# Optimization experiments

Measured on AMD Instinct MI355X. Metric: run time of the kernel, lower is better.

Reference implementation:

```python
import jax, jax.numpy as jnp
import numpy as np

WH, WW = 8, 8          # window size
SH, SW = 4, 4          # shift size
HEADS = 8

def _rel_pos_index(wh, ww):
    # static Swin relative-position index, identical to the torch __init__ math
    coords = np.stack(np.meshgrid(np.arange(wh), np.arange(ww), indexing='ij')).reshape(2, -1)
    rel = (coords[:, :, None] - coords[:, None, :]).transpose(1, 2, 0)
    rel[..., 0] += wh - 1
    rel[..., 1] += ww - 1
    rel[..., 0] *= 2 * ww - 1
    return jnp.asarray(rel.sum(-1))  # (N, N) int

REL_IDX = _rel_pos_index(WH, WW)

def _ln(x, w, b, eps=1e-5):
    m = x.mean(-1, keepdims=True)
    v = ((x - m) ** 2).mean(-1, keepdims=True)
    return (x - m) * jax.lax.rsqrt(v + eps) * w + b

def _lin(x, w, b):  # torch Linear convention: w is (out, in)
    return jnp.einsum('...i,oi->...o', x, w) + b

def _partition(x):
    B, H, W, C = x.shape
    x = x.reshape(B, H // WH, WH, W // WW, WW, C).transpose(0, 1, 3, 2, 4, 5)
    return x.reshape(-1, WH * WW, C)  # (B*nW, N, C)

def _reverse(w, B, H, W):
    C = w.shape[-1]
    x = w.reshape(B, H // WH, W // WW, WH, WW, C).transpose(0, 1, 3, 2, 4, 5)
    return x.reshape(B, H, W, C)

def _win_attn(q_in, kv_in, qw, qb, kvw, kvb, pw, pb, table, mask):
    B_, N1, C = q_in.shape
    N2 = kv_in.shape[1]
    hd = C // HEADS
    scale = hd ** -0.5
    q = _lin(q_in, qw, qb).reshape(B_, N1, HEADS, hd).transpose(0, 2, 1, 3)
    kv = _lin(kv_in, kvw, kvb).reshape(B_, N2, 2, HEADS, hd).transpose(2, 0, 3, 1, 4)
    k, v = kv[0], kv[1]
    attn = jnp.einsum('bhqd,bhkd->bhqk', q * scale, k)               # (B_, H, N1, N2)
    bias = table[REL_IDX.reshape(-1)].reshape(N1, N2, HEADS).transpose(2, 0, 1)
    attn = attn + bias[None]
    nW = mask.shape[0]
    attn = attn.reshape(B_ // nW, nW, HEADS, N1, N2) + mask[None, :, None]
    attn = jax.nn.softmax(attn.reshape(B_, HEADS, N1, N2), axis=-1)
    out = jnp.einsum('bhqk,bhkd->bhqd', attn, v).transpose(0, 2, 1, 3).reshape(B_, N1, C)
    return _lin(out, pw, pb)

def reference(x, attn_kv, mask_q, mask_qkv,
              n1w, n1b, n2w, n2b, n3w, n3b, nkvw, nkvb,
              a1_qw, a1_qb, a1_kvw, a1_kvb, a1_pw, a1_pb, a1_tab,
              a2_qw, a2_qb, a2_kvw, a2_kvb, a2_pw, a2_pb, a2_tab,
              fc1w, fc1b, fc2w, fc2b):
    B, H, W, C = x.shape  # H,W divisible by window -> pad is a no-op; shift active
    # --- shifted-window self attention ---
    shortcut = x
    h = jnp.roll(_ln(x, n1w, n1b), (-SH, -SW), axis=(1, 2))
    w = _win_attn(_partition(h), _partition(h), a1_qw, a1_qb, a1_kvw, a1_kvb,
                  a1_pw, a1_pb, a1_tab, mask_q)
    x = shortcut + jnp.roll(_reverse(w, B, H, W), (SH, SW), axis=(1, 2))
    # --- shifted-window cross attention ---
    shortcut = x
    hq = jnp.roll(_ln(x, n2w, n2b), (-SH, -SW), axis=(1, 2))
    hkv = jnp.roll(_ln(attn_kv, nkvw, nkvb), (-SH, -SW), axis=(1, 2))
    w = _win_attn(_partition(hq), _partition(hkv), a2_qw, a2_qb, a2_kvw, a2_kvb,
                  a2_pw, a2_pb, a2_tab, mask_qkv)
    x = shortcut + jnp.roll(_reverse(w, B, H, W), (SH, SW), axis=(1, 2))
    # --- MLP ---
    h = _ln(x, n3w, n3b)
    h = _lin(jax.nn.gelu(_lin(h, fc1w, fc1b), approximate=False), fc2w, fc2b)
    return x + h

def setup_inputs() -> dict:
    key = jax.random.key(0)
    ks = jax.random.split(key, 20)
    B, H, W, C = 2, 256, 256, 256
    nW = (H // WH) * (W // WW)
    N = WH * WW
    hid = 4 * C
    tab = (2 * WH - 1) * (2 * WW - 1)
    rn = lambda k, s, sd=0.02: jax.random.normal(k, s, jnp.float32) * sd
    shift_mask = lambda k: jnp.where(jax.random.uniform(k, (nW, N, N)) > 0.1, 0.0, -100.0).astype(jnp.float32)
    return dict(
        x=jax.random.normal(ks[0], (B, H, W, C), jnp.float32),
        attn_kv=jax.random.normal(ks[1], (B, H, W, C), jnp.float32),
        mask_q=shift_mask(ks[2]), mask_qkv=shift_mask(ks[3]),
        n1w=jnp.ones((C,)), n1b=jnp.zeros((C,)),
        n2w=jnp.ones((C,)), n2b=jnp.zeros((C,)),
        n3w=jnp.ones((C,)), n3b=jnp.zeros((C,)),
        nkvw=jnp.ones((C,)), nkvb=jnp.zeros((C,)),
        a1_qw=rn(ks[4], (C, C)), a1_qb=jnp.zeros((C,)),
        a1_kvw=rn(ks[5], (2 * C, C)), a1_kvb=jnp.zeros((2 * C,)),
        a1_pw=rn(ks[6], (C, C)), a1_pb=jnp.zeros((C,)),
        a1_tab=rn(ks[7], (tab, HEADS)),
        a2_qw=rn(ks[8], (C, C)), a2_qb=jnp.zeros((C,)),
        a2_kvw=rn(ks[9], (2 * C, C)), a2_kvb=jnp.zeros((2 * C,)),
        a2_pw=rn(ks[10], (C, C)), a2_pb=jnp.zeros((C,)),
        a2_tab=rn(ks[11], (tab, HEADS)),
        fc1w=rn(ks[12], (hid, C)), fc1b=jnp.zeros((hid,)),
        fc2w=rn(ks[13], (C, hid)), fc2b=jnp.zeros((C,)),
    )
```

## Files before the change

kernel.cpp:

```cpp
#include <hip/hip_runtime.h>
#include <math.h>

typedef __attribute__((ext_vector_type(8))) short short8;
typedef __attribute__((ext_vector_type(4))) float f32x4;

__device__ __forceinline__ unsigned short f2bf(float f) {
  unsigned u = __float_as_uint(f);
  u += 0x7FFFu + ((u >> 16) & 1u);
  return (unsigned short)(u >> 16);
}
__device__ __forceinline__ float bf2f(unsigned short h) {
  return __uint_as_float(((unsigned)h) << 16);
}

static constexpr unsigned OFF_WQKV1 = 0;
static constexpr unsigned OFF_BQKV1 = 393216;
static constexpr unsigned OFF_WQ2   = 396288;
static constexpr unsigned OFF_BQ2   = 527360;
static constexpr unsigned OFF_WKV2  = 528384;
static constexpr unsigned OFF_BKV2  = 790528;
static constexpr unsigned OFF_WP1   = 792576;
static constexpr unsigned OFF_BP1   = 923648;
static constexpr unsigned OFF_WP2   = 924672;
static constexpr unsigned OFF_BP2   = 1055744;
static constexpr unsigned OFF_WFC1  = 1056768;
static constexpr unsigned OFF_BFC1  = 1581056;
static constexpr unsigned OFF_WFC2  = 1585152;
static constexpr unsigned OFF_BFC2  = 2109440;
static constexpr unsigned OFF_BIAS1 = 2110464;
static constexpr unsigned OFF_BIAS2 = 2241536;

static constexpr size_t OFF_X1  = 4194304;
static constexpr size_t OFF_QKV = OFF_X1  + 134217728ull;
static constexpr size_t OFF_KV2 = OFF_QKV + 67108864ull;
static constexpr size_t OFF_HB  = OFF_QKV + 201326592ull;
static constexpr size_t OFF_HA  = OFF_HB  + 67108864ull;

__global__ __launch_bounds__(256) void prep_kernel(
    const float* __restrict__ a1_qw, const float* __restrict__ a1_qb,
    const float* __restrict__ a1_kvw, const float* __restrict__ a1_kvb,
    const float* __restrict__ a1_pw, const float* __restrict__ a1_pb,
    const float* __restrict__ a1_tab,
    const float* __restrict__ a2_qw, const float* __restrict__ a2_qb,
    const float* __restrict__ a2_kvw, const float* __restrict__ a2_kvb,
    const float* __restrict__ a2_pw, const float* __restrict__ a2_pb,
    const float* __restrict__ a2_tab,
    const float* __restrict__ fc1w, const float* __restrict__ fc1b,
    const float* __restrict__ fc2w, const float* __restrict__ fc2b,
    char* __restrict__ ws)
{
  int idx = blockIdx.x * 256 + threadIdx.x;
  const float SC = 0.17677669529663687f;
  if (idx < 196608) {
    int o = idx >> 8, c = idx & 255;
    float v = (o < 256) ? a1_qw[o * 256 + c] * SC : a1_kvw[(o - 256) * 256 + c];
    ((unsigned short*)(ws + OFF_WQKV1))[idx] = f2bf(v);
    return;
  }
  idx -= 196608;
  if (idx < 768) {
    float v = (idx < 256) ? a1_qb[idx] * SC : a1_kvb[idx - 256];
    ((float*)(ws + OFF_BQKV1))[idx] = v; return;
  }
  idx -= 768;
  if (idx < 65536) { ((unsigned short*)(ws + OFF_WQ2))[idx] = f2bf(a2_qw[idx] * SC); return; }
  idx -= 65536;
  if (idx < 256)   { ((float*)(ws + OFF_BQ2))[idx] = a2_qb[idx] * SC; return; }
  idx -= 256;
  if (idx < 131072){ ((unsigned short*)(ws + OFF_WKV2))[idx] = f2bf(a2_kvw[idx]); return; }
  idx -= 131072;
  if (idx < 512)   { ((float*)(ws + OFF_BKV2))[idx] = a2_kvb[idx]; return; }
  idx -= 512;
  if (idx < 65536) { ((unsigned short*)(ws + OFF_WP1))[idx] = f2bf(a1_pw[idx]); return; }
  idx -= 65536;
  if (idx < 256)   { ((float*)(ws + OFF_BP1))[idx] = a1_pb[idx]; return; }
  idx -= 256;
  if (idx < 65536) { ((unsigned short*)(ws + OFF_WP2))[idx] = f2bf(a2_pw[idx]); return; }
  idx -= 65536;
  if (idx < 256)   { ((float*)(ws + OFF_BP2))[idx] = a2_pb[idx]; return; }
  idx -= 256;
  if (idx < 262144){ ((unsigned short*)(ws + OFF_WFC1))[idx] = f2bf(fc1w[idx]); return; }
  idx -= 262144;
  if (idx < 1024)  { ((float*)(ws + OFF_BFC1))[idx] = fc1b[idx]; return; }
  idx -= 1024;
  if (idx < 262144){ ((unsigned short*)(ws + OFF_WFC2))[idx] = f2bf(fc2w[idx]); return; }
  idx -= 262144;
  if (idx < 256)   { ((float*)(ws + OFF_BFC2))[idx] = fc2b[idx]; return; }
  idx -= 256;
  if (idx < 32768) {
    int h = idx >> 12, r = idx & 4095;
    int i = r >> 6, j = r & 63;
    int rel = ((i >> 3) - (j >> 3) + 7) * 15 + ((i & 7) - (j & 7) + 7);
    ((float*)(ws + OFF_BIAS1))[idx] = a1_tab[rel * 8 + h];
    return;
  }
  idx -= 32768;
  if (idx < 32768) {
    int h = idx >> 12, r = idx & 4095;
    int i = r >> 6, j = r & 63;
    int rel = ((i >> 3) - (j >> 3) + 7) * 15 + ((i & 7) - (j & 7) + 7);
    ((float*)(ws + OFF_BIAS2))[idx] = a2_tab[rel * 8 + h];
  }
}

template<int SHIFTED>
__global__ __launch_bounds__(256)
void ln_kernel(const float* __restrict__ in, const float* __restrict__ gw,
               const float* __restrict__ gb, unsigned short* __restrict__ out)
{
  const int token = blockIdx.x * 4 + (threadIdx.x >> 6);
  const int lane  = threadIdx.x & 63;
  const float4 v = *(const float4*)&in[token * 256 + lane * 4];
  float s  = v.x + v.y + v.z + v.w;
  float sq = v.x * v.x + v.y * v.y + v.z * v.z + v.w * v.w;
  #pragma unroll
  for (int m = 1; m < 64; m <<= 1) { s += __shfl_xor(s, m, 64); sq += __shfl_xor(sq, m, 64); }
  const float mean = s * 0.00390625f;
  const float var  = sq * 0.00390625f - mean * mean;
  const float rstd = rsqrtf(var + 1e-5f);
  const float4 wv = *(const float4*)&gw[lane * 4];
  const float4 bv = *(const float4*)&gb[lane * 4];
  int orow;
  if (SHIFTED) {
    const int bb = token >> 16;
    const int h  = (token >> 8) & 255;
    const int w  = token & 255;
    const int hs  = (h - 4) & 255;
    const int wsn = (w - 4) & 255;
    orow = (((bb << 10) + ((hs >> 3) << 5) + (wsn >> 3)) << 6) + ((hs & 7) << 3) + (wsn & 7);
  } else {
    orow = token;
  }
  ushort4 o;
  o.x = f2bf((v.x - mean) * rstd * wv.x + bv.x);
  o.y = f2bf((v.y - mean) * rstd * wv.y + bv.y);
  o.z = f2bf((v.z - mean) * rstd * wv.z + bv.z);
  o.w = f2bf((v.w - mean) * rstd * wv.w + bv.w);
  *(ushort4*)&out[orow * 256 + lane * 4] = o;
}

template<int MODE>
__global__ __launch_bounds__(256)
void gemm_bt(const unsigned short* __restrict__ A, const unsigned short* __restrict__ W,
             const float* __restrict__ bias, int M, int N, int K,
             unsigned short* __restrict__ outB, float* outF, const float* resF)
{
  __shared__ unsigned short As[128 * 64];
  __shared__ unsigned short Bs[128 * 64];
  const int tid  = threadIdx.x;
  const int lane = tid & 63;
  const int wv   = tid >> 6;
  const int n0 = blockIdx.x * 128;
  const int m0 = blockIdx.y * 128;
  const int wm = (wv >> 1) * 64;
  const int wn = (wv & 1) * 64;
  const int lr = lane & 15;
  const int lk = (lane >> 4) * 8;

  f32x4 acc[4][4] = {};

  for (int k0 = 0; k0 < K; k0 += 64) {
    #pragma unroll
    for (int s = 0; s < 4; s++) {
      const int u = tid + s * 256;
      const int r = u >> 3;
      const int c = (u & 7) * 8;
      const int sw = (r & 7) << 3;
      *(short8*)&As[(r * 64 + c) ^ sw] = *(const short8*)&A[(m0 + r) * K + k0 + c];
      *(short8*)&Bs[(r * 64 + c) ^ sw] = *(const short8*)&W[(n0 + r) * K + k0 + c];
    }
    __syncthreads();
    #pragma unroll
    for (int kk = 0; kk < 64; kk += 32) {
      short8 af[4], bf[4];
      #pragma unroll
      for (int i = 0; i < 4; i++) {
        const int ra = wm + i * 16 + lr;
        const int rb = wn + i * 16 + lr;
        af[i] = *(const short8*)&As[(ra * 64 + kk + lk) ^ ((ra & 7) << 3)];
        bf[i] = *(const short8*)&Bs[(rb * 64 + kk + lk) ^ ((rb & 7) << 3)];
      }
      #pragma unroll
      for (int i = 0; i < 4; i++)
        #pragma unroll
        for (int j = 0; j < 4; j++)
          acc[i][j] = __builtin_amdgcn_mfma_f32_16x16x32_bf16(af[i], bf[j], acc[i][j], 0, 0, 0);
    }
    __syncthreads();
  }

  #pragma unroll
  for (int j = 0; j < 4; j++) {
    const int col = n0 + wn + j * 16 + lr;
    const float bv = bias[col];
    #pragma unroll
    for (int i = 0; i < 4; i++) {
      #pragma unroll
      for (int r = 0; r < 4; r++) {
        const int row = m0 + wm + i * 16 + (lane >> 4) * 4 + r;
        float v = acc[i][j][r] + bv;
        if (MODE == 0) {
          outB[row * N + col] = f2bf(v);
        } else if (MODE == 1) {
          float g = 0.5f * v * (1.0f + erff(v * 0.70710678118654752f));
          outB[row * N + col] = f2bf(g);
        } else if (MODE == 2) {
          const int i6 = row & 63, wn_ = row >> 6;
          const int bb = wn_ >> 10, wi = wn_ & 1023;
          const int hs  = ((wi >> 5) << 3) + (i6 >> 3);
          const int wsn = ((wi & 31) << 3) + (i6 & 7);
          const int hh = (hs + 4) & 255, ww = (wsn + 4) & 255;
          const int nat = (bb << 16) + (hh << 8) + ww;
          outF[nat * 256 + col] = resF[nat * 256 + col] + v;
        } else {
          outF[row * N + col] = resF[row * N + col] + v;
        }
      }
    }
  }
}

__global__ __launch_bounds__(256)
void attn_kernel(const unsigned short* __restrict__ Qm, int sq,
                 const unsigned short* __restrict__ Km,
                 const unsigned short* __restrict__ Vm, int skv,
                 const float* __restrict__ mask, const float* __restrict__ biasT,
                 unsigned short* __restrict__ outO)
{
  __shared__ unsigned short Kl[64 * 256];
  __shared__ unsigned short Vl[64 * 256];
  const int win = blockIdx.x;
  const int wi  = win & 1023;
  const int tid = threadIdx.x;
  const int t = tid & 63;
  const int g = tid >> 6;

  for (int u = tid; u < 2048; u += 256) {
    const int j = u >> 5;
    const int c = (u & 31) * 8;
    *(short8*)&Kl[j * 256 + c] = *(const short8*)&Km[(win * 64 + j) * skv + c];
    *(short8*)&Vl[j * 256 + c] = *(const short8*)&Vm[(win * 64 + j) * skv + c];
  }
  __syncthreads();

  const float* mrow = &mask[wi * 4096 + t * 64];

  #pragma unroll
  for (int hh = 0; hh < 2; hh++) {
    const int h = g * 2 + hh;
    float qr[32];
    const unsigned short* qp = &Qm[(win * 64 + t) * sq + h * 32];
    #pragma unroll
    for (int c = 0; c < 4; c++) {
      const short8 qv = *(const short8*)&qp[c * 8];
      #pragma unroll
      for (int e = 0; e < 8; e++) qr[c * 8 + e] = bf2f((unsigned short)qv[e]);
    }
    const float* brow = &biasT[h * 4096 + t * 64];
    float s[64];
    #pragma unroll
    for (int j = 0; j < 64; j++) {
      const unsigned short* kp = &Kl[j * 256 + h * 32];
      float a = 0.f;
      #pragma unroll
      for (int c = 0; c < 4; c++) {
        const short8 k8 = *(const short8*)&kp[c * 8];
        #pragma unroll
        for (int e = 0; e < 8; e++) a = fmaf(qr[c * 8 + e], bf2f((unsigned short)k8[e]), a);
      }
      s[j] = a + brow[j] + mrow[j];
    }
    float mx = -1e30f;
    #pragma unroll
    for (int j = 0; j < 64; j++) mx = fmaxf(mx, s[j]);
    float sum = 0.f;
    #pragma unroll
    for (int j = 0; j < 64; j++) { const float e = __expf(s[j] - mx); s[j] = e; sum += e; }
    const float inv = 1.f / sum;
    float o[32];
    #pragma unroll
    for (int d = 0; d < 32; d++) o[d] = 0.f;
    #pragma unroll
    for (int j = 0; j < 64; j++) {
      const float p = s[j];
      const unsigned short* vp = &Vl[j * 256 + h * 32];
      #pragma unroll
      for (int c = 0; c < 4; c++) {
        const short8 v8 = *(const short8*)&vp[c * 8];
        #pragma unroll
        for (int e = 0; e < 8; e++) o[c * 8 + e] = fmaf(p, bf2f((unsigned short)v8[e]), o[c * 8 + e]);
      }
    }
    unsigned short* op = &outO[(win * 64 + t) * 256 + h * 32];
    #pragma unroll
    for (int c = 0; c < 4; c++) {
      short8 ov;
      #pragma unroll
      for (int e = 0; e < 8; e++) ov[e] = (short)f2bf(o[c * 8 + e] * inv);
      *(short8*)&op[c * 8] = ov;
    }
  }
}

extern "C" void kernel_launch(void* const* d_in, const int* in_sizes, int n_in,
                              void* d_out, int out_size, void* d_ws, size_t ws_size,
                              hipStream_t stream)
{
  const float* x       = (const float*)d_in[0];
  const float* akv     = (const float*)d_in[1];
  const float* mask_q  = (const float*)d_in[2];
  const float* mask_kv = (const float*)d_in[3];
  const float* n1w = (const float*)d_in[4];
  const float* n1b = (const float*)d_in[5];
  const float* n2w = (const float*)d_in[6];
  const float* n2b = (const float*)d_in[7];
  const float* n3w = (const float*)d_in[8];
  const float* n3b = (const float*)d_in[9];
  const float* nkvw = (const float*)d_in[10];
  const float* nkvb = (const float*)d_in[11];

  char* ws = (char*)d_ws;
  const unsigned short* WQKV1 = (const unsigned short*)(ws + OFF_WQKV1);
  const float*          BQKV1 = (const float*)(ws + OFF_BQKV1);
  const unsigned short* WQ2   = (const unsigned short*)(ws + OFF_WQ2);
  const float*          BQ2   = (const float*)(ws + OFF_BQ2);
  const unsigned short* WKV2  = (const unsigned short*)(ws + OFF_WKV2);
  const float*          BKV2  = (const float*)(ws + OFF_BKV2);
  const unsigned short* WP1   = (const unsigned short*)(ws + OFF_WP1);
  const float*          BP1   = (const float*)(ws + OFF_BP1);
  const unsigned short* WP2   = (const unsigned short*)(ws + OFF_WP2);
  const float*          BP2   = (const float*)(ws + OFF_BP2);
  const unsigned short* WFC1  = (const unsigned short*)(ws + OFF_WFC1);
  const float*          BFC1  = (const float*)(ws + OFF_BFC1);
  const unsigned short* WFC2  = (const unsigned short*)(ws + OFF_WFC2);
  const float*          BFC2  = (const float*)(ws + OFF_BFC2);
  const float* BIAS1 = (const float*)(ws + OFF_BIAS1);
  const float* BIAS2 = (const float*)(ws + OFF_BIAS2);

  float*          x1  = (float*)(ws + OFF_X1);
  unsigned short* qkv = (unsigned short*)(ws + OFF_QKV);
  unsigned short* kv2 = (unsigned short*)(ws + OFF_KV2);
  unsigned short* hB  = (unsigned short*)(ws + OFF_HB);
  unsigned short* hA  = (unsigned short*)(ws + OFF_HA);
  float* out = (float*)d_out;

  prep_kernel<<<4365, 256, 0, stream>>>(
      (const float*)d_in[12], (const float*)d_in[13], (const float*)d_in[14], (const float*)d_in[15],
      (const float*)d_in[16], (const float*)d_in[17], (const float*)d_in[18],
      (const float*)d_in[19], (const float*)d_in[20], (const float*)d_in[21], (const float*)d_in[22],
      (const float*)d_in[23], (const float*)d_in[24], (const float*)d_in[25],
      (const float*)d_in[26], (const float*)d_in[27], (const float*)d_in[28], (const float*)d_in[29],
      ws);

  ln_kernel<1><<<32768, 256, 0, stream>>>(x, n1w, n1b, hA);
  gemm_bt<0><<<dim3(6, 1024), 256, 0, stream>>>(hA, WQKV1, BQKV1, 131072, 768, 256, qkv, nullptr, nullptr);
  attn_kernel<<<2048, 256, 0, stream>>>(qkv, 768, qkv + 256, qkv + 512, 768, mask_q, BIAS1, hA);
  gemm_bt<2><<<dim3(2, 1024), 256, 0, stream>>>(hA, WP1, BP1, 131072, 256, 256, nullptr, x1, x);

  ln_kernel<1><<<32768, 256, 0, stream>>>(x1, n2w, n2b, hA);
  ln_kernel<1><<<32768, 256, 0, stream>>>(akv, nkvw, nkvb, hB);
  gemm_bt<0><<<dim3(2, 1024), 256, 0, stream>>>(hA, WQ2, BQ2, 131072, 256, 256, qkv, nullptr, nullptr);
  gemm_bt<0><<<dim3(4, 1024), 256, 0, stream>>>(hB, WKV2, BKV2, 131072, 512, 256, kv2, nullptr, nullptr);
  attn_kernel<<<2048, 256, 0, stream>>>(qkv, 256, kv2, kv2 + 256, 512, mask_kv, BIAS2, hA);
  gemm_bt<2><<<dim3(2, 1024), 256, 0, stream>>>(hA, WP2, BP2, 131072, 256, 256, nullptr, out, x1);

  ln_kernel<0><<<32768, 256, 0, stream>>>(out, n3w, n3b, hA);
  gemm_bt<1><<<dim3(8, 1024), 256, 0, stream>>>(hA, WFC1, BFC1, 131072, 1024, 256, qkv, nullptr, nullptr);
  gemm_bt<3><<<dim3(2, 1024), 256, 0, stream>>>(qkv, WFC2, BFC2, 131072, 256, 1024, nullptr, out, out);
}
```

Baseline: 2.386 ms.

## Use MFMA for window attention and direct global-to-LDS loads in GEMM

Rewrites the window attention kernel so QK^T and PV run on bf16 MFMA instructions instead of per-thread scalar FMA loops. Heads are processed in two halves, with K staged via global_load_lds, V transposed into swizzled LDS, and softmax done with cross-lane shuffles and P written to LDS as bf16. The GEMM tile loads switch to direct global-to-LDS loads with an XOR swizzle applied on the global side, and indexing is widened to size_t. Quantizing P to bf16 adds some rounding error, and the extra LDS and sync per half may limit occupancy.

```diff
diff --git a/kernel.cpp b/kernel.cpp
--- a/kernel.cpp
+++ b/kernel.cpp
@@ -11,6 +11,10 @@
 }
 __device__ __forceinline__ float bf2f(unsigned short h) {
   return __uint_as_float(((unsigned)h) << 16);
+}
+__device__ __forceinline__ void gload_lds16(const unsigned short* g, unsigned short* l) {
+  __builtin_amdgcn_global_load_lds((const __attribute__((address_space(1))) void*)g,
+                                   (__attribute__((address_space(3))) void*)l, 16, 0, 0);
 }
 
 static constexpr unsigned OFF_WQKV1 = 0;
@@ -110,7 +114,7 @@
 {
   const int token = blockIdx.x * 4 + (threadIdx.x >> 6);
   const int lane  = threadIdx.x & 63;
-  const float4 v = *(const float4*)&in[token * 256 + lane * 4];
+  const float4 v = *(const float4*)&in[(size_t)token * 256 + lane * 4];
   float s  = v.x + v.y + v.z + v.w;
   float sq = v.x * v.x + v.y * v.y + v.z * v.z + v.w * v.w;
   #pragma unroll
@@ -136,7 +140,7 @@
   o.y = f2bf((v.y - mean) * rstd * wv.y + bv.y);
   o.z = f2bf((v.z - mean) * rstd * wv.z + bv.z);
   o.w = f2bf((v.w - mean) * rstd * wv.w + bv.w);
-  *(ushort4*)&out[orow * 256 + lane * 4] = o;
+  *(ushort4*)&out[(size_t)orow * 256 + lane * 4] = o;
 }
 
 template<int MODE>
@@ -145,8 +149,8 @@
              const float* __restrict__ bias, int M, int N, int K,
              unsigned short* __restrict__ outB, float* outF, const float* resF)
 {
-  __shared__ unsigned short As[128 * 64];
-  __shared__ unsigned short Bs[128 * 64];
+  __shared__ __align__(16) unsigned short As[128 * 64];
+  __shared__ __align__(16) unsigned short Bs[128 * 64];
   const int tid  = threadIdx.x;
   const int lane = tid & 63;
   const int wv   = tid >> 6;
@@ -157,17 +161,17 @@
   const int lr = lane & 15;
   const int lk = (lane >> 4) * 8;
 
+  const int r8  = lane >> 3;
+  const int gch = (lane & 7) ^ r8;
+
   f32x4 acc[4][4] = {};
 
   for (int k0 = 0; k0 < K; k0 += 64) {
     #pragma unroll
     for (int s = 0; s < 4; s++) {
-      const int u = tid + s * 256;
-      const int r = u >> 3;
-      const int c = (u & 7) * 8;
-      const int sw = (r & 7) << 3;
-      *(short8*)&As[(r * 64 + c) ^ sw] = *(const short8*)&A[(m0 + r) * K + k0 + c];
-      *(short8*)&Bs[(r * 64 + c) ^ sw] = *(const short8*)&W[(n0 + r) * K + k0 + c];
+      const int rbase = wv * 32 + s * 8;
+      gload_lds16(&A[(size_t)(m0 + rbase + r8) * K + k0 + gch * 8], &As[rbase * 64]);
+      gload_lds16(&W[(size_t)(n0 + rbase + r8) * K + k0 + gch * 8], &Bs[rbase * 64]);
     }
     __syncthreads();
     #pragma unroll
@@ -200,20 +204,20 @@
         const int row = m0 + wm + i * 16 + (lane >> 4) * 4 + r;
         float v = acc[i][j][r] + bv;
         if (MODE == 0) {
-          outB[row * N + col] = f2bf(v);
+          outB[(size_t)row * N + col] = f2bf(v);
         } else if (MODE == 1) {
-          float g = 0.5f * v * (1.0f + erff(v * 0.70710678118654752f));
-          outB[row * N + col] = f2bf(g);
+          float gl = 0.5f * v * (1.0f + erff(v * 0.70710678118654752f));
+          outB[(size_t)row * N + col] = f2bf(gl);
         } else if (MODE == 2) {
           const int i6 = row & 63, wn_ = row >> 6;
           const int bb = wn_ >> 10, wi = wn_ & 1023;
           const int hs  = ((wi >> 5) << 3) + (i6 >> 3);
           const int wsn = ((wi & 31) << 3) + (i6 & 7);
           const int hh = (hs + 4) & 255, ww = (wsn + 4) & 255;
-          const int nat = (bb << 16) + (hh << 8) + ww;
+          const size_t nat = ((size_t)bb << 16) + (hh << 8) + ww;
           outF[nat * 256 + col] = resF[nat * 256 + col] + v;
         } else {
-          outF[row * N + col] = resF[row * N + col] + v;
+          outF[(size_t)row * N + col] = resF[(size_t)row * N + col] + v;
         }
       }
     }
@@ -227,78 +231,124 @@
                  const float* __restrict__ mask, const float* __restrict__ biasT,
                  unsigned short* __restrict__ outO)
 {
-  __shared__ unsigned short Kl[64 * 256];
-  __shared__ unsigned short Vl[64 * 256];
+  __shared__ __align__(16) unsigned short Kh[64 * 128];
+  __shared__ __align__(16) unsigned short Vth[128 * 64];
+  __shared__ __align__(16) unsigned short Ps[4 * 64 * 64];
+
   const int win = blockIdx.x;
   const int wi  = win & 1023;
   const int tid = threadIdx.x;
-  const int t = tid & 63;
-  const int g = tid >> 6;
-
-  for (int u = tid; u < 2048; u += 256) {
-    const int j = u >> 5;
-    const int c = (u & 31) * 8;
-    *(short8*)&Kl[j * 256 + c] = *(const short8*)&Km[(win * 64 + j) * skv + c];
-    *(short8*)&Vl[j * 256 + c] = *(const short8*)&Vm[(win * 64 + j) * skv + c];
-  }
-  __syncthreads();
-
-  const float* mrow = &mask[wi * 4096 + t * 64];
-
-  #pragma unroll
-  for (int hh = 0; hh < 2; hh++) {
-    const int h = g * 2 + hh;
-    float qr[32];
-    const unsigned short* qp = &Qm[(win * 64 + t) * sq + h * 32];
-    #pragma unroll
-    for (int c = 0; c < 4; c++) {
-      const short8 qv = *(const short8*)&qp[c * 8];
-      #pragma unroll
-      for (int e = 0; e < 8; e++) qr[c * 8 + e] = bf2f((unsigned short)qv[e]);
-    }
-    const float* brow = &biasT[h * 4096 + t * 64];
-    float s[64];
-    #pragma unroll
-    for (int j = 0; j < 64; j++) {
-      const unsigned short* kp = &Kl[j * 256 + h * 32];
-      float a = 0.f;
-      #pragma unroll
-      for (int c = 0; c < 4; c++) {
-        const short8 k8 = *(const short8*)&kp[c * 8];
-        #pragma unroll
-        for (int e = 0; e < 8; e++) a = fmaf(qr[c * 8 + e], bf2f((unsigned short)k8[e]), a);
-      }
-      s[j] = a + brow[j] + mrow[j];
-    }
-    float mx = -1e30f;
-    #pragma unroll
-    for (int j = 0; j < 64; j++) mx = fmaxf(mx, s[j]);
-    float sum = 0.f;
-    #pragma unroll
-    for (int j = 0; j < 64; j++) { const float e = __expf(s[j] - mx); s[j] = e; sum += e; }
-    const float inv = 1.f / sum;
-    float o[32];
-    #pragma unroll
-    for (int d = 0; d < 32; d++) o[d] = 0.f;
-    #pragma unroll
-    for (int j = 0; j < 64; j++) {
-      const float p = s[j];
-      const unsigned short* vp = &Vl[j * 256 + h * 32];
-      #pragma unroll
-      for (int c = 0; c < 4; c++) {
-        const short8 v8 = *(const short8*)&vp[c * 8];
-        #pragma unroll
-        for (int e = 0; e < 8; e++) o[c * 8 + e] = fmaf(p, bf2f((unsigned short)v8[e]), o[c * 8 + e]);
-      }
-    }
-    unsigned short* op = &outO[(win * 64 + t) * 256 + h * 32];
-    #pragma unroll
-    for (int c = 0; c < 4; c++) {
-      short8 ov;
-      #pragma unroll
-      for (int e = 0; e < 8; e++) ov[e] = (short)f2bf(o[c * 8 + e] * inv);
-      *(short8*)&op[c * 8] = ov;
-    }
+  const int lane = tid & 63;
+  const int wv  = tid >> 6;
+  const int lr = lane & 15;
+  const int g  = lane >> 4;
+  unsigned short* Pw = &Ps[wv * 4096];
+
+  for (int half = 0; half < 2; half++) {
+    {
+      const int r_off = g;
+      const int ch    = lane & 15;
+      #pragma unroll
+      for (int s = 0; s < 4; s++) {
+        const int row = wv * 16 + s * 4 + r_off;
+        const int sch = ch ^ (row & 7);
+        gload_lds16(&Km[(size_t)(win * 64 + row) * skv + half * 128 + sch * 8],
+                    &Kh[(wv * 16 + s * 4) * 128]);
+      }
+    }
+    #pragma unroll
+    for (int it = 0; it < 4; it++) {
+      const int slot = tid + it * 256;
+      const int tok = slot >> 4;
+      const int ch  = slot & 15;
+      const short8 v8 = *(const short8*)&Vm[(size_t)(win * 64 + tok) * skv + half * 128 + ch * 8];
+      #pragma unroll
+      for (int es = 0; es < 8; es++) {
+        const int e  = (es + ch) & 7;
+        const int fr = ch * 8 + e;
+        Vth[fr * 64 + (((tok >> 3) ^ (fr & 7)) << 3) + (tok & 7)] = (unsigned short)v8[e];
+      }
+    }
+    __syncthreads();
+
+    const int h = half * 4 + wv;
+    short8 af[4];
+    #pragma unroll
+    for (int i = 0; i < 4; i++)
+      af[i] = *(const short8*)&Qm[(size_t)(win * 64 + i * 16 + lr) * sq + h * 32 + g * 8];
+    f32x4 acc[4][4] = {};
+    #pragma unroll
+    for (int j = 0; j < 4; j++) {
+      const int row = j * 16 + lr;
+      const int chn = ((h & 3) * 4 + g) ^ (row & 7);
+      const short8 bf = *(const short8*)&Kh[row * 128 + chn * 8];
+      #pragma unroll
+      for (int i = 0; i < 4; i++)
+        acc[i][j] = __builtin_amdgcn_mfma_f32_16x16x32_bf16(af[i], bf, acc[i][j], 0, 0, 0);
+    }
+
+    const float* bh = &biasT[h * 4096];
+    const float* mh = &mask[(size_t)wi * 4096];
+    #pragma unroll
+    for (int i = 0; i < 4; i++) {
+      #pragma unroll
+      for (int r = 0; r < 4; r++) {
+        const int row = i * 16 + g * 4 + r;
+        #pragma unroll
+        for (int j = 0; j < 4; j++) {
+          const int col = j * 16 + lr;
+          acc[i][j][r] += bh[row * 64 + col] + mh[row * 64 + col];
+        }
+        float m4 = fmaxf(fmaxf(acc[i][0][r], acc[i][1][r]), fmaxf(acc[i][2][r], acc[i][3][r]));
+        #pragma unroll
+        for (int mk = 1; mk < 16; mk <<= 1) m4 = fmaxf(m4, __shfl_xor(m4, mk, 64));
+        float sum = 0.f;
+        #pragma unroll
+        for (int j = 0; j < 4; j++) {
+          const float e = __expf(acc[i][j][r] - m4);
+          acc[i][j][r] = e; sum += e;
+        }
+        #pragma unroll
+        for (int mk = 1; mk < 16; mk <<= 1) sum += __shfl_xor(sum, mk, 64);
+        const float inv = 1.f / sum;
+        #pragma unroll
+        for (int j = 0; j < 4; j++) {
+          const int col = j * 16 + lr;
+          Pw[row * 64 + (((col >> 3) ^ (row & 7)) << 3) + (col & 7)] = f2bf(acc[i][j][r] * inv);
+        }
+      }
+    }
+
+    f32x4 o[4][2] = {};
+    #pragma unroll
+    for (int kk = 0; kk < 2; kk++) {
+      short8 bv[2];
+      #pragma unroll
+      for (int jj = 0; jj < 2; jj++) {
+        const int frow = (h & 3) * 32 + jj * 16 + lr;
+        const int chn = (kk * 4 + g) ^ (frow & 7);
+        bv[jj] = *(const short8*)&Vth[frow * 64 + chn * 8];
+      }
+      #pragma unroll
+      for (int i = 0; i < 4; i++) {
+        const int prow = i * 16 + lr;
+        const int chn = (kk * 4 + g) ^ (prow & 7);
+        const short8 pa = *(const short8*)&Pw[prow * 64 + chn * 8];
+        #pragma unroll
+        for (int jj = 0; jj < 2; jj++)
+          o[i][jj] = __builtin_amdgcn_mfma_f32_16x16x32_bf16(pa, bv[jj], o[i][jj], 0, 0, 0);
+      }
+    }
+    #pragma unroll
+    for (int i = 0; i < 4; i++)
+      #pragma unroll
+      for (int jj = 0; jj < 2; jj++)
+        #pragma unroll
+        for (int r = 0; r < 4; r++) {
+          const int row = i * 16 + g * 4 + r;
+          outO[(size_t)(win * 64 + row) * 256 + h * 32 + jj * 16 + lr] = f2bf(o[i][jj][r]);
+        }
+    __syncthreads();
   }
 }
 
```

After: 2.083 ms. 12.7% less time.
